# Kernel tuning notes

Measured on AMD Instinct MI355X. Metric: run time of the kernel, lower is better.

## Reference

```python
import jax, jax.numpy as jnp
import numpy as np

N = 100000; E = 800000; IN_DIM = 32; HID = 64; HEADS = 4; HEAD_DIM = HID // HEADS; L = 3; G = 128

def setup_inputs() -> dict:
    key = jax.random.key(0)
    ks = jax.random.split(key, 12)
    nrm = lambda k, shape: jax.random.normal(k, shape, jnp.float32) * 0.05
    return {
        "x": jax.random.normal(ks[0], (N, IN_DIM), jnp.float32),
        "edge_index": jax.random.randint(ks[1], (2, E), 0, N),
        "edge_attr": jax.random.normal(ks[2], (E, 1), jnp.float32),
        "batch": jnp.sort(jax.random.randint(ks[3], (N,), 0, G)),
        "in_W": nrm(ks[4], (IN_DIM, HID)), "in_b": jnp.zeros((HID,), jnp.float32),
        "in_ln_g": jnp.ones((HID,), jnp.float32), "in_ln_b": jnp.zeros((HID,), jnp.float32),
        "W_qkv": nrm(ks[5], (L, 3, HID, HID)), "b_qkv": jnp.zeros((L, 3, HID), jnp.float32),
        "W_edge": nrm(ks[6], (L, 1, HID)),
        "W_skip": nrm(ks[7], (L, HID, HID)), "b_skip": jnp.zeros((L, HID), jnp.float32),
        "W_beta": nrm(ks[8], (L, 3 * HID)),
        "ln_g": jnp.ones((L, HID), jnp.float32), "ln_b": jnp.zeros((L, HID), jnp.float32),
        "r1_W": nrm(ks[9], (2 * HID, HID)), "r1_b": jnp.zeros((HID,), jnp.float32),
        "r2_W": nrm(ks[10], (HID, HID // 2)), "r2_b": jnp.zeros((HID // 2,), jnp.float32),
        "r3_W": nrm(ks[11], (HID // 2, 1)), "r3_b": jnp.zeros((1,), jnp.float32),
    }

def _layer_norm(x, g, b, eps=1e-5):
    mu = x.mean(-1, keepdims=True)
    var = ((x - mu) ** 2).mean(-1, keepdims=True)
    return (x - mu) * jax.lax.rsqrt(var + eps) * g + b

def _gelu(x):
    return jax.nn.gelu(x, approximate=False)  # matches torch F.gelu default (erf)

def _forward(x, edge_attr, in_W, in_b, in_ln_g, in_ln_b, W_qkv, b_qkv, W_edge,
             W_skip, b_skip, W_beta, ln_g, ln_b, r1_W, r1_b, r2_W, r2_b, r3_W, r3_b,
             edge_index, batch):
    src, dst = edge_index[0], edge_index[1]  # message flows src -> dst
    n = x.shape[0]
    h = _layer_norm(_gelu(x @ in_W + in_b), in_ln_g, in_ln_b)
    scale = 1.0 / jnp.sqrt(jnp.float32(HEAD_DIM))
    for l in range(L):
        res = h
        q = (h @ W_qkv[l, 0] + b_qkv[l, 0]).reshape(n, HEADS, HEAD_DIM)
        k = (h @ W_qkv[l, 1] + b_qkv[l, 1]).reshape(n, HEADS, HEAD_DIM)
        v = (h @ W_qkv[l, 2] + b_qkv[l, 2]).reshape(n, HEADS, HEAD_DIM)
        e = (edge_attr @ W_edge[l]).reshape(-1, HEADS, HEAD_DIM)  # [E,H,C]
        ke = k[src] + e
        alpha = jnp.einsum("ehc,ehc->eh", q[dst], ke) * scale      # [E,H]
        amax = jax.ops.segment_max(alpha, dst, num_segments=n)
        ex = jnp.exp(alpha - amax[dst])
        den = jax.ops.segment_sum(ex, dst, num_segments=n)
        alpha = ex / (den[dst] + 1e-16)                            # PyG softmax eps
        msg = alpha[..., None] * (v[src] + e)
        out = jax.ops.segment_sum(msg, dst, num_segments=n).reshape(n, HID)
        x_r = h @ W_skip[l] + b_skip[l]
        beta = jax.nn.sigmoid(jnp.concatenate([out, x_r, out - x_r], -1) @ W_beta[l])  # [N]
        out = beta[:, None] * x_r + (1.0 - beta[:, None]) * out
        h = _layer_norm(_gelu(out) + res, ln_g[l], ln_b[l])
    cnt = jax.ops.segment_sum(jnp.ones((n,), h.dtype), batch, num_segments=G)
    gmean = jax.ops.segment_sum(h, batch, num_segments=G) / jnp.maximum(cnt, 1.0)[:, None]
    gmax = jax.ops.segment_max(h, batch, num_segments=G)
    rep = jnp.concatenate([gmean, gmax], -1)  # [G, 2*HID]
    rep = _gelu(rep @ r1_W + r1_b)
    rep = _gelu(rep @ r2_W + r2_b)
    return (rep @ r3_W + r3_b).reshape(-1)

def reference(x, edge_index, edge_attr, batch, in_W, in_b, in_ln_g, in_ln_b,
              W_qkv, b_qkv, W_edge, W_skip, b_skip, W_beta, ln_g, ln_b,
              r1_W, r1_b, r2_W, r2_b, r3_W, r3_b):
    return _forward(x, edge_attr, in_W, in_b, in_ln_g, in_ln_b, W_qkv, b_qkv, W_edge,
                    W_skip, b_skip, W_beta, ln_g, ln_b, r1_W, r1_b, r2_W, r2_b, r3_W, r3_b,
                    edge_index, batch)
```

## Files before the change

kernel.cpp:

```cpp
#include <hip/hip_runtime.h>
#include <hip/hip_fp16.h>
#include <math.h>
#include <float.h>

#define LAYERS 3
#define NGRAPH 128
#define NPB 1024
#define NBMAX 256

typedef __attribute__((ext_vector_type(8))) short bf16x8;
typedef __attribute__((ext_vector_type(4))) float f32x4;

union bfr { int4 i; bf16x8 b; };

__device__ __forceinline__ float gelu_f(float x) {
    return 0.5f * x * (1.0f + erff(x * 0.70710678118654752440f));
}

template <int CTRL, int RMASK>
__device__ __forceinline__ float dpp_add(float x) {
    int t = __builtin_amdgcn_update_dpp(0, __float_as_int(x), CTRL, RMASK, 0xF, false);
    return x + __int_as_float(t);
}

__device__ __forceinline__ float sum16(float v) {
    v = dpp_add<0xB1, 0xF>(v);
    v = dpp_add<0x4E, 0xF>(v);
    v = dpp_add<0x141, 0xF>(v);
    v = dpp_add<0x140, 0xF>(v);
    return v;
}

__device__ __forceinline__ unsigned int f2mono(float f) {
    unsigned int u = __float_as_uint(f);
    return (u & 0x80000000u) ? ~u : (u | 0x80000000u);
}
__device__ __forceinline__ float mono2f(unsigned int u) {
    return (u & 0x80000000u) ? __uint_as_float(u ^ 0x80000000u)
                             : __uint_as_float(~u);
}

__device__ __forceinline__ float2 h2f2(int bits) {
    __half2 h = *reinterpret_cast<__half2*>(&bits);
    return __half22float2(h);
}

__device__ __forceinline__ void cvt_frag(const float4& f0, const float4& f1,
                                         bf16x8& hi, bf16x8& lo) {
    float ff[8] = {f0.x, f0.y, f0.z, f0.w, f1.x, f1.y, f1.z, f1.w};
#pragma unroll
    for (int j = 0; j < 8; j++) {
        unsigned u = __float_as_uint(ff[j]);
        hi[j] = (short)(u >> 16);
        float hf = __uint_as_float(u & 0xFFFF0000u);
        lo[j] = (short)(__float_as_uint(ff[j] - hf) >> 16);
    }
}

__device__ __forceinline__ f32x4 mm3(const bf16x8& ahi, const bf16x8& alo,
                                     const int4* __restrict__ pk, int tile,
                                     int lane, f32x4 acc) {
    bfr bh, bl;
    bh.i = pk[tile * 128 + lane];
    bl.i = pk[tile * 128 + 64 + lane];
    acc = __builtin_amdgcn_mfma_f32_16x16x32_bf16(alo, bh.b, acc, 0, 0, 0);
    acc = __builtin_amdgcn_mfma_f32_16x16x32_bf16(ahi, bl.b, acc, 0, 0, 0);
    acc = __builtin_amdgcn_mfma_f32_16x16x32_bf16(ahi, bh.b, acc, 0, 0, 0);
    return acc;
}

__global__ __launch_bounds__(256) void k_cvt(
    const float* __restrict__ in_W, const float* __restrict__ W_skip,
    const float* __restrict__ W_qkv, int4* __restrict__ pk_in,
    int4* __restrict__ pk_skip, int4* __restrict__ pk_qkv) {
    int w = (blockIdx.x * 256 + threadIdx.x) >> 6;
    if (w >= 100) return;
    int lane = threadIdx.x & 63;
    const float* src;
    int4* dst;
    int kt, jt, qkvmode = 0;
    if (w < 4) {
        kt = 0; jt = w;
        src = in_W;
        dst = pk_in + w * 128;
    } else {
        int l = (w - 4) >> 5, r = (w - 4) & 31;
        if (r < 8) {
            kt = r & 1; jt = r >> 1;
            src = W_skip + l * 4096;
            dst = pk_skip + (l * 8 + r) * 128;
        } else {
            int tq = r - 8;
            kt = tq & 1; jt = tq >> 1;
            src = W_qkv + l * 12288;
            dst = pk_qkv + (l * 24 + tq) * 128;
            qkvmode = 1;
        }
    }
    int c = jt * 16 + (lane & 15);
    int koff = kt * 32 + (lane >> 4) * 8;
    unsigned hi[8], lo[8];
#pragma unroll
    for (int j = 0; j < 8; j++) {
        int k = koff + j;
        float f = qkvmode ? src[(c >> 6) * 4096 + k * 64 + (c & 63)]
                          : src[k * 64 + c];
        unsigned u = __float_as_uint(f);
        hi[j] = u >> 16;
        float hf = __uint_as_float(u & 0xFFFF0000u);
        lo[j] = __float_as_uint(f - hf) >> 16;
    }
    int4 H, L;
    H.x = hi[0] | (hi[1] << 16); H.y = hi[2] | (hi[3] << 16);
    H.z = hi[4] | (hi[5] << 16); H.w = hi[6] | (hi[7] << 16);
    L.x = lo[0] | (lo[1] << 16); L.y = lo[2] | (lo[3] << 16);
    L.z = lo[4] | (lo[5] << 16); L.w = lo[6] | (lo[7] << 16);
    dst[lane] = H;
    dst[64 + lane] = L;
}

__global__ __launch_bounds__(256) void k_hist(const int* __restrict__ dst,
                                              int* __restrict__ deg, int E) {
    int e = blockIdx.x * 256 + threadIdx.x;
    if (e < E) atomicAdd(&deg[dst[e]], 1);
}

__global__ __launch_bounds__(256) void k_scan1(const int* __restrict__ deg,
                                               int* __restrict__ excl,
                                               int* __restrict__ bsum, int n) {
    __shared__ int s[256];
    int t = threadIdx.x;
    int i = blockIdx.x * 256 + t;
    int v = (i < n) ? deg[i] : 0;
    s[t] = v;
    __syncthreads();
    for (int off = 1; off < 256; off <<= 1) {
        int a = (t >= off) ? s[t - off] : 0;
        __syncthreads();
        s[t] += a;
        __syncthreads();
    }
    if (i < n) excl[i] = s[t] - v;
    if (t == 255) bsum[blockIdx.x] = s[255];
}

__global__ __launch_bounds__(512) void k_scan2(int* __restrict__ bsum, int nb) {
    __shared__ int s[512];
    int t = threadIdx.x;
    int v = (t < nb) ? bsum[t] : 0;
    s[t] = v;
    __syncthreads();
    for (int off = 1; off < 512; off <<= 1) {
        int a = (t >= off) ? s[t - off] : 0;
        __syncthreads();
        s[t] += a;
        __syncthreads();
    }
    if (t < nb) bsum[t] = s[t] - v;
}

__global__ __launch_bounds__(256) void k_scan3(const int* __restrict__ excl,
                                               const int* __restrict__ bsum,
                                               int* __restrict__ row,
                                               int* __restrict__ cursor,
                                               int* __restrict__ gcurb,
                                               int n, int E) {
    int i = blockIdx.x * 256 + threadIdx.x;
    if (i < n) {
        int r = excl[i] + bsum[blockIdx.x];
        row[i] = r;
        cursor[i] = r;
        if ((i & (NPB - 1)) == 0) gcurb[i >> 10] = r;
    }
    if (blockIdx.x == 0 && threadIdx.x == 0) row[n] = E;
}

__global__ __launch_bounds__(256) void k_bucket(
    const int* __restrict__ src, const int* __restrict__ dst,
    const float* __restrict__ ea, int* __restrict__ gcurb,
    int2* __restrict__ mid, int E, int nbkt) {
    __shared__ int cnt[NBMAX], base_[NBMAX];
    int tile = blockIdx.x * 4096;
    for (int i = threadIdx.x; i < nbkt; i += 256) cnt[i] = 0;
    __syncthreads();
    int d[16];
#pragma unroll
    for (int j = 0; j < 16; j++) {
        int e = tile + j * 256 + threadIdx.x;
        d[j] = -1;
        if (e < E) {
            d[j] = dst[e];
            atomicAdd(&cnt[d[j] >> 10], 1);
        }
    }
    __syncthreads();
    for (int i = threadIdx.x; i < nbkt; i += 256) {
        base_[i] = atomicAdd(&gcurb[i], cnt[i]);
        cnt[i] = 0;
    }
    __syncthreads();
#pragma unroll
    for (int j = 0; j < 16; j++) {
        int e = tile + j * 256 + threadIdx.x;
        if (e < E) {
            int b = d[j] >> 10;
            int p = base_[b] + atomicAdd(&cnt[b], 1);
            mid[p] = make_int2(src[e] | ((d[j] & (NPB - 1)) << 20),
                               __float_as_int(ea[e]));
        }
    }
}

__global__ __launch_bounds__(256) void k_local(
    const int* __restrict__ row, int* __restrict__ cursor,
    const int2* __restrict__ mid, int2* __restrict__ ep, int n) {
    int b = blockIdx.x;
    int n0 = b << 10;
    int n1 = min(n, n0 + NPB);
    int ebeg = row[n0], eend = row[n1];
    for (int e = ebeg + blockIdx.y * 256 + threadIdx.x; e < eend;
         e += 256 * gridDim.y) {
        int2 m = mid[e];
        int dn = n0 + ((m.x >> 20) & (NPB - 1));
        int p = atomicAdd(&cursor[dn], 1);
        ep[p] = make_int2(m.x & 0xFFFFF, m.y);
    }
}

__device__ __forceinline__ int kv_idx(int m, int cc) {
    return (cc >> 2) * 8 + (m - 1) * 4 + (cc & 3);
}

__global__ __launch_bounds__(256) void k_in_qkv(
    const float* __restrict__ x, const int4* __restrict__ pk_in,
    const float* __restrict__ b, const float* __restrict__ g,
    const float* __restrict__ be, const int4* __restrict__ pk_qkv,
    const float* __restrict__ bn, float* __restrict__ h,
    __half* __restrict__ q, __half* __restrict__ kvout, int n) {
    __shared__ float lds[4][1088];
    int lane = threadIdx.x & 63, wid = threadIdx.x >> 6;
    int nb = (blockIdx.x * 4 + wid) * 16;
    if (nb >= n) return;
    int g16 = lane >> 4, c16 = lane & 15;
    int arow = min(nb + c16, n - 1);
    const float* xp = x + (size_t)arow * 32 + g16 * 8;
    float4 f0 = *(const float4*)xp;
    float4 f1 = *(const float4*)(xp + 4);
    bf16x8 ahi, alo;
    cvt_frag(f0, f1, ahi, alo);
    float gv[4][4];
#pragma unroll
    for (int jt = 0; jt < 4; jt++) {
        f32x4 a = {0.f, 0.f, 0.f, 0.f};
        a = mm3(ahi, alo, pk_in, jt, lane, a);
        float bb = b[jt * 16 + c16];
#pragma unroll
        for (int r = 0; r < 4; r++) gv[jt][r] = gelu_f(a[r] + bb);
    }
    float gl[4], bel[4];
#pragma unroll
    for (int jt = 0; jt < 4; jt++) {
        gl[jt] = g[jt * 16 + c16];
        bel[jt] = be[jt * 16 + c16];
    }
    float hreg[4][4];
#pragma unroll
    for (int r = 0; r < 4; r++) {
        float s = gv[0][r] + gv[1][r] + gv[2][r] + gv[3][r];
        float mu = sum16(s) * (1.0f / 64.0f);
        float vs = 0.f;
#pragma unroll
        for (int jt = 0; jt < 4; jt++) {
            float d = gv[jt][r] - mu;
            vs += d * d;
        }
        float var = sum16(vs) * (1.0f / 64.0f);
        float rs = rsqrtf(var + 1e-5f);
#pragma unroll
        for (int jt = 0; jt < 4; jt++)
            hreg[jt][r] = (gv[jt][r] - mu) * rs * gl[jt] + bel[jt];
    }
#pragma unroll
    for (int jt = 0; jt < 4; jt++)
#pragma unroll
        for (int r = 0; r < 4; r++) {
            int nd = nb + g16 * 4 + r;
            if (nd < n) h[(size_t)nd * 64 + jt * 16 + c16] = hreg[jt][r];
            lds[wid][(g16 * 4 + r) * 68 + jt * 16 + c16] = hreg[jt][r];
        }
    bf16x8 qahi[2], qalo[2];
#pragma unroll
    for (int kt = 0; kt < 2; kt++) {
        const float* lp = &lds[wid][c16 * 68 + kt * 32 + g16 * 8];
        float4 t0 = *(const float4*)lp;
        float4 t1 = *(const float4*)(lp + 4);
        cvt_frag(t0, t1, qahi[kt], qalo[kt]);
    }
#pragma unroll
    for (int jt = 0; jt < 12; jt++) {
        f32x4 a = {0.f, 0.f, 0.f, 0.f};
#pragma unroll
        for (int kt = 0; kt < 2; kt++) a = mm3(qahi[kt], qalo[kt], pk_qkv, jt * 2 + kt, lane, a);
        int c = jt * 16 + c16;
        float bias = bn[c];
        int m = c >> 6, cc = c & 63;
#pragma unroll
        for (int r = 0; r < 4; r++) {
            int nd = nb + g16 * 4 + r;
            if (nd < n) {
                float val = a[r] + bias;
                if (m == 0) q[(size_t)nd * 64 + cc] = __float2half(val);
                else kvout[(size_t)nd * 128 + kv_idx(m, cc)] = __float2half(val);
            }
        }
    }
}

__global__ __launch_bounds__(256) void k_attn(
    const __half* __restrict__ q, const __half* __restrict__ kv,
    const int* __restrict__ row, const int2* __restrict__ ep,
    const float* __restrict__ We, float* __restrict__ out, int n) {
    int lane = threadIdx.x & 63;
    int node = blockIdx.x * 4 + (threadIdx.x >> 6);
    if (node >= n) return;
    int g = lane >> 4;
    int c16 = lane & 15;
    int2 qb = *(const int2*)(q + (size_t)node * 64 + c16 * 4);
    float2 q01 = h2f2(qb.x), q23 = h2f2(qb.y);
    float4 wv = *(const float4*)(We + c16 * 4);
    int beg = row[node], end = row[node + 1];
    float den = 0.f;
    float4 acc = {0.f, 0.f, 0.f, 0.f};
    for (int pos = beg; pos < end; pos += 8) {
        int idx0 = pos + g, idx1 = pos + 4 + g;
        bool v0 = idx0 < end, v1 = idx1 < end;
        int2 pr0 = ep[v0 ? idx0 : beg];
        int2 pr1 = ep[v1 ? idx1 : beg];
        float a0 = __int_as_float(pr0.y), a1 = __int_as_float(pr1.y);
        int4 kb0 = *(const int4*)(kv + (size_t)pr0.x * 128 + c16 * 8);
        int4 kb1 = *(const int4*)(kv + (size_t)pr1.x * 128 + c16 * 8);
        {
            float2 k01 = h2f2(kb0.x), k23 = h2f2(kb0.y);
            float2 v01 = h2f2(kb0.z), v23 = h2f2(kb0.w);
            float p = q01.x * fmaf(a0, wv.x, k01.x) + q01.y * fmaf(a0, wv.y, k01.y) +
                      q23.x * fmaf(a0, wv.z, k23.x) + q23.y * fmaf(a0, wv.w, k23.y);
            p = dpp_add<0xB1, 0xF>(p);
            p = dpp_add<0x4E, 0xF>(p);
            float ex = v0 ? __expf(fminf(p * 0.25f, 60.f)) : 0.f;
            den += ex;
            acc.x = fmaf(ex, fmaf(a0, wv.x, v01.x), acc.x);
            acc.y = fmaf(ex, fmaf(a0, wv.y, v01.y), acc.y);
            acc.z = fmaf(ex, fmaf(a0, wv.z, v23.x), acc.z);
            acc.w = fmaf(ex, fmaf(a0, wv.w, v23.y), acc.w);
        }
        {
            float2 k01 = h2f2(kb1.x), k23 = h2f2(kb1.y);
            float2 v01 = h2f2(kb1.z), v23 = h2f2(kb1.w);
            float p = q01.x * fmaf(a1, wv.x, k01.x) + q01.y * fmaf(a1, wv.y, k01.y) +
                      q23.x * fmaf(a1, wv.z, k23.x) + q23.y * fmaf(a1, wv.w, k23.y);
            p = dpp_add<0xB1, 0xF>(p);
            p = dpp_add<0x4E, 0xF>(p);
            float ex = v1 ? __expf(fminf(p * 0.25f, 60.f)) : 0.f;
            den += ex;
            acc.x = fmaf(ex, fmaf(a1, wv.x, v01.x), acc.x);
            acc.y = fmaf(ex, fmaf(a1, wv.y, v01.y), acc.y);
            acc.z = fmaf(ex, fmaf(a1, wv.z, v23.x), acc.z);
            acc.w = fmaf(ex, fmaf(a1, wv.w, v23.y), acc.w);
        }
    }
#pragma unroll
    for (int mask = 16; mask <= 32; mask <<= 1) {
        den += __shfl_xor(den, mask, 64);
        acc.x += __shfl_xor(acc.x, mask, 64);
        acc.y += __shfl_xor(acc.y, mask, 64);
        acc.z += __shfl_xor(acc.z, mask, 64);
        acc.w += __shfl_xor(acc.w, mask, 64);
    }
    if (g == 0) {
        float inv = 1.0f / (den + 1e-16f);
        float4 o = {acc.x * inv, acc.y * inv, acc.z * inv, acc.w * inv};
        *(float4*)(out + (size_t)node * 64 + c16 * 4) = o;
    }
}

template <int DO_QKV>
__global__ __launch_bounds__(256) void k_node_qkv(
    float* __restrict__ h, const float* __restrict__ o_in,
    const int4* __restrict__ pk_skip, const float* __restrict__ bs,
    const float* __restrict__ Wb, const float* __restrict__ lg,
    const float* __restrict__ lb, const int4* __restrict__ pk_qkv,
    const float* __restrict__ bn, __half* __restrict__ q,
    __half* __restrict__ kvout, const int* __restrict__ batch,
    float* __restrict__ gsum, unsigned int* __restrict__ gmaxu,
    float* __restrict__ cnt, int n) {
    __shared__ float lds[4][DO_QKV ? 1088 : 4];
    int lane = threadIdx.x & 63, wid = threadIdx.x >> 6;
    int nb = (blockIdx.x * 4 + wid) * 16;
    if (nb >= n) return;
    int g16 = lane >> 4, c16 = lane & 15;
    bf16x8 ahi[2], alo[2];
    int arow = min(nb + c16, n - 1);
#pragma unroll
    for (int kt = 0; kt < 2; kt++) {
        const float* hp = h + (size_t)arow * 64 + kt * 32 + g16 * 8;
        float4 f0 = *(const float4*)hp;
        float4 f1 = *(const float4*)(hp + 4);
        cvt_frag(f0, f1, ahi[kt], alo[kt]);
    }
    float xr[4][4];
#pragma unroll
    for (int jt = 0; jt < 4; jt++) {
        f32x4 a = {0.f, 0.f, 0.f, 0.f};
#pragma unroll
        for (int kt = 0; kt < 2; kt++) a = mm3(ahi[kt], alo[kt], pk_skip, jt * 2 + kt, lane, a);
        float bias = bs[jt * 16 + c16];
#pragma unroll
        for (int r = 0; r < 4; r++) xr[jt][r] = a[r] + bias;
    }
    float ov[4][4], hold[4][4];
#pragma unroll
    for (int jt = 0; jt < 4; jt++)
#pragma unroll
        for (int r = 0; r < 4; r++) {
            int nd = min(nb + g16 * 4 + r, n - 1);
            ov[jt][r] = o_in[(size_t)nd * 64 + jt * 16 + c16];
            hold[jt][r] = h[(size_t)nd * 64 + jt * 16 + c16];
        }
    float wb0[4], wb1[4], wb2[4], lgv[4], lbv[4];
#pragma unroll
    for (int jt = 0; jt < 4; jt++) {
        int c = jt * 16 + c16;
        wb0[jt] = Wb[c]; wb1[jt] = Wb[64 + c]; wb2[jt] = Wb[128 + c];
        lgv[jt] = lg[c]; lbv[jt] = lb[c];
    }
    float hnew[4][4];
#pragma unroll
    for (int r = 0; r < 4; r++) {
        float cbs = 0.f;
#pragma unroll
        for (int jt = 0; jt < 4; jt++)
            cbs += ov[jt][r] * wb0[jt] + xr[jt][r] * wb1[jt] +
                   (ov[jt][r] - xr[jt][r]) * wb2[jt];
        float cb = sum16(cbs);
        float beta = 1.0f / (1.0f + expf(-cb));
        float gvr[4], s = 0.f;
#pragma unroll
        for (int jt = 0; jt < 4; jt++) {
            float o2 = fmaf(beta, xr[jt][r] - ov[jt][r], ov[jt][r]);
            gvr[jt] = gelu_f(o2) + hold[jt][r];
            s += gvr[jt];
        }
        float mu = sum16(s) * (1.0f / 64.0f);
        float vs = 0.f;
#pragma unroll
        for (int jt = 0; jt < 4; jt++) {
            float d = gvr[jt] - mu;
            vs += d * d;
        }
        float var = sum16(vs) * (1.0f / 64.0f);
        float rs = rsqrtf(var + 1e-5f);
#pragma unroll
        for (int jt = 0; jt < 4; jt++)
            hnew[jt][r] = (gvr[jt] - mu) * rs * lgv[jt] + lbv[jt];
    }
    if (DO_QKV) {
#pragma unroll
        for (int jt = 0; jt < 4; jt++)
#pragma unroll
            for (int r = 0; r < 4; r++) {
                int nd = nb + g16 * 4 + r;
                if (nd < n) h[(size_t)nd * 64 + jt * 16 + c16] = hnew[jt][r];
                lds[wid][(g16 * 4 + r) * 68 + jt * 16 + c16] = hnew[jt][r];
            }
        bf16x8 qahi[2], qalo[2];
#pragma unroll
        for (int kt = 0; kt < 2; kt++) {
            const float* lp = &lds[wid][c16 * 68 + kt * 32 + g16 * 8];
            float4 t0 = *(const float4*)lp;
            float4 t1 = *(const float4*)(lp + 4);
            cvt_frag(t0, t1, qahi[kt], qalo[kt]);
        }
#pragma unroll
        for (int jt = 0; jt < 12; jt++) {
            f32x4 a = {0.f, 0.f, 0.f, 0.f};
#pragma unroll
            for (int kt = 0; kt < 2; kt++) a = mm3(qahi[kt], qalo[kt], pk_qkv, jt * 2 + kt, lane, a);
            int c = jt * 16 + c16;
            float bias = bn[c];
            int m = c >> 6, cc = c & 63;
#pragma unroll
            for (int r = 0; r < 4; r++) {
                int nd = nb + g16 * 4 + r;
                if (nd < n) {
                    float val = a[r] + bias;
                    if (m == 0) q[(size_t)nd * 64 + cc] = __float2half(val);
                    else kvout[(size_t)nd * 128 + kv_idx(m, cc)] = __float2half(val);
                }
            }
        }
    } else {
        int gid[4];
        int g0 = batch[nb];
        bool ok = (nb + 15 < n);
#pragma unroll
        for (int r = 0; r < 4; r++)
            gid[r] = batch[min(nb + g16 * 4 + r, n - 1)];
        bool uni = ok && __all(gid[0] == g0 && gid[1] == g0 &&
                               gid[2] == g0 && gid[3] == g0);
        if (uni) {
            float s[4], mx[4];
#pragma unroll
            for (int jt = 0; jt < 4; jt++) {
                s[jt] = hnew[jt][0] + hnew[jt][1] + hnew[jt][2] + hnew[jt][3];
                mx[jt] = fmaxf(fmaxf(hnew[jt][0], hnew[jt][1]),
                               fmaxf(hnew[jt][2], hnew[jt][3]));
            }
#pragma unroll
            for (int mask = 16; mask <= 32; mask <<= 1) {
#pragma unroll
                for (int jt = 0; jt < 4; jt++) {
                    s[jt] += __shfl_xor(s[jt], mask, 64);
                    mx[jt] = fmaxf(mx[jt], __shfl_xor(mx[jt], mask, 64));
                }
            }
            if (g16 == 0) {
#pragma unroll
                for (int jt = 0; jt < 4; jt++) {
                    int ch = jt * 16 + c16;
                    atomicAdd(&gsum[g0 * 64 + ch], s[jt]);
                    atomicMax(&gmaxu[g0 * 64 + ch], f2mono(mx[jt]));
                }
            }
            if (lane == 0) atomicAdd(&cnt[g0], 16.0f);
        } else {
#pragma unroll
            for (int r = 0; r < 4; r++) {
                int nd = nb + g16 * 4 + r;
                if (nd >= n) continue;
#pragma unroll
                for (int jt = 0; jt < 4; jt++) {
                    int ch = jt * 16 + c16;
                    atomicAdd(&gsum[gid[r] * 64 + ch], hnew[jt][r]);
                    atomicMax(&gmaxu[gid[r] * 64 + ch], f2mono(hnew[jt][r]));
                }
                if (c16 == 0) atomicAdd(&cnt[gid[r]], 1.0f);
            }
        }
    }
}

__global__ void k_final(const float* __restrict__ gsum,
                        const unsigned int* __restrict__ gmax,
                        const float* __restrict__ cnt,
                        const float* __restrict__ W1, const float* __restrict__ b1,
                        const float* __restrict__ W2, const float* __restrict__ b2,
                        const float* __restrict__ W3, const float* __restrict__ b3,
                        float* __restrict__ out) {
    int g = blockIdx.x;
    int lane = threadIdx.x;
    __shared__ float rep[128];
    __shared__ float t1[64];
    __shared__ float t2[32];
    float c = fmaxf(cnt[g], 1.0f);
    rep[lane] = gsum[g * 64 + lane] / c;
    rep[64 + lane] = mono2f(gmax[g * 64 + lane]);
    __syncthreads();
    float a = b1[lane];
#pragma unroll 8
    for (int i = 0; i < 128; i++) a = fmaf(rep[i], W1[i * 64 + lane], a);
    t1[lane] = gelu_f(a);
    __syncthreads();
    if (lane < 32) {
        float a2 = b2[lane];
#pragma unroll 8
        for (int i = 0; i < 64; i++) a2 = fmaf(t1[i], W2[i * 32 + lane], a2);
        t2[lane] = gelu_f(a2);
    }
    __syncthreads();
    if (lane < 32) {
        float p = t2[lane] * W3[lane];
#pragma unroll
        for (int o = 16; o > 0; o >>= 1) p += __shfl_xor(p, o, 64);
        if (lane == 0) out[g] = p + b3[0];
    }
}

extern "C" void kernel_launch(void* const* d_in, const int* in_sizes, int n_in,
                              void* d_out, int out_size, void* d_ws,
                              size_t ws_size, hipStream_t stream) {
    const float* x      = (const float*)d_in[0];
    const int*   eidx   = (const int*)d_in[1];
    const float* ea     = (const float*)d_in[2];
    const int*   batch  = (const int*)d_in[3];
    const float* in_W   = (const float*)d_in[4];
    const float* in_b   = (const float*)d_in[5];
    const float* in_lng = (const float*)d_in[6];
    const float* in_lnb = (const float*)d_in[7];
    const float* W_qkv  = (const float*)d_in[8];
    const float* b_qkv  = (const float*)d_in[9];
    const float* W_edge = (const float*)d_in[10];
    const float* W_skip = (const float*)d_in[11];
    const float* b_skip = (const float*)d_in[12];
    const float* W_beta = (const float*)d_in[13];
    const float* ln_g   = (const float*)d_in[14];
    const float* ln_b   = (const float*)d_in[15];
    const float* r1_W   = (const float*)d_in[16];
    const float* r1_b   = (const float*)d_in[17];
    const float* r2_W   = (const float*)d_in[18];
    const float* r2_b   = (const float*)d_in[19];
    const float* r3_W   = (const float*)d_in[20];
    const float* r3_b   = (const float*)d_in[21];

    int n = in_sizes[0] / 32;
    int E = in_sizes[2];
    const int* src = eidx;
    const int* dst = eidx + E;

    char* ws = (char*)d_ws;
    size_t off = 0;
    auto alloc = [&](size_t bytes) -> void* {
        void* p = ws + off;
        off = (off + bytes + 255) & ~(size_t)255;
        return p;
    };
    float* h    = (float*)alloc((size_t)n * 64 * 4);
    __half* qh  = (__half*)alloc((size_t)n * 64 * 2);
    __half* kvh = (__half*)alloc((size_t)n * 128 * 2);
    float* oacc = (float*)alloc((size_t)n * 64 * 4);
    int* deg    = (int*)alloc((size_t)n * 4);
    int* excl   = (int*)alloc((size_t)n * 4);
    int* bsum   = (int*)alloc(512 * 4);
    int* row    = (int*)alloc((size_t)(n + 1) * 4);
    int* cursor = (int*)alloc((size_t)n * 4);
    int* gcurb  = (int*)alloc(NBMAX * 4);
    int2* mid   = (int2*)alloc((size_t)E * 8);
    int2* ep    = (int2*)alloc((size_t)E * 8);
    int4* pk_in   = (int4*)alloc(4 * 128 * 16);
    int4* pk_skip = (int4*)alloc(3 * 8 * 128 * 16);
    int4* pk_qkv  = (int4*)alloc((size_t)3 * 24 * 128 * 16);
    float* gsum = (float*)alloc((NGRAPH * 64 * 2 + NGRAPH) * 4);
    unsigned int* gmaxu = (unsigned int*)(gsum + NGRAPH * 64);
    float* cnt  = gsum + NGRAPH * 128;

    int nb4 = (n + 3) / 4;
    int nb64 = (n + 63) / 64;
    int nbs = (n + 255) / 256;
    int ebs = (E + 255) / 256;
    int nbkt = (n + NPB - 1) >> 10;

    k_cvt<<<25, 256, 0, stream>>>(in_W, W_skip, W_qkv, pk_in, pk_skip, pk_qkv);
    hipMemsetAsync(deg, 0, (size_t)n * 4, stream);
    hipMemsetAsync(gsum, 0, (NGRAPH * 64 * 2 + NGRAPH) * 4, stream);
    k_hist<<<ebs, 256, 0, stream>>>(dst, deg, E);
    k_scan1<<<nbs, 256, 0, stream>>>(deg, excl, bsum, n);
    k_scan2<<<1, 512, 0, stream>>>(bsum, nbs);
    k_scan3<<<nbs, 256, 0, stream>>>(excl, bsum, row, cursor, gcurb, n, E);
    k_bucket<<<(E + 4095) / 4096, 256, 0, stream>>>(src, dst, ea, gcurb, mid, E, nbkt);
    k_local<<<dim3(nbkt, 4), 256, 0, stream>>>(row, cursor, mid, ep, n);

    k_in_qkv<<<nb64, 256, 0, stream>>>(x, pk_in, in_b, in_lng, in_lnb,
                                       pk_qkv, b_qkv, h, qh, kvh, n);

    for (int l = 0; l < LAYERS; l++) {
        k_attn<<<nb4, 256, 0, stream>>>(qh, kvh, row, ep, W_edge + l * 64, oacc, n);
        if (l + 1 < LAYERS) {
            k_node_qkv<1><<<nb64, 256, 0, stream>>>(
                h, oacc, pk_skip + l * 8 * 128, b_skip + l * 64,
                W_beta + l * 192, ln_g + l * 64, ln_b + l * 64,
                pk_qkv + (size_t)(l + 1) * 24 * 128, b_qkv + (size_t)(l + 1) * 192,
                qh, kvh, nullptr, nullptr, nullptr, nullptr, n);
        } else {
            k_node_qkv<0><<<nb64, 256, 0, stream>>>(
                h, oacc, pk_skip + l * 8 * 128, b_skip + l * 64,
                W_beta + l * 192, ln_g + l * 64, ln_b + l * 64,
                nullptr, nullptr, nullptr, nullptr,
                batch, gsum, gmaxu, cnt, n);
        }
    }

    k_final<<<NGRAPH, 64, 0, stream>>>(gsum, gmaxu, cnt, r1_W, r1_b, r2_W, r2_b,
                                       r3_W, r3_b, (float*)d_out);
}
```

Before: 381.1 us.

## Process 4 nodes per 64-thread block in node kernels and hoist edge term in attention

The node-side kernels (input projection and per-layer skip/beta/LN/QKV) now launch one 64-thread block per 4 nodes instead of 256-thread blocks covering 64 nodes. Only 4 of the 16 MFMA rows carry real nodes, and results are staged through LDS so that h, q and kv are written with coalesced vector stores instead of scattered half stores. This spreads the node work over many more small blocks and cleans up the store pattern, but three quarters of the MFMA rows do redundant work and an extra block-level sync is added. Separately, the attention kernel folds the edge-attribute term algebraically: q·W_edge is computed once per node and the sum of exp-weighted edge attributes is accumulated, which removes per-edge FMAs.

```diff
diff --git a/kernel.cpp b/kernel.cpp
--- a/kernel.cpp
+++ b/kernel.cpp
@@ -28,6 +28,11 @@
     v = dpp_add<0x4E, 0xF>(v);
     v = dpp_add<0x141, 0xF>(v);
     v = dpp_add<0x140, 0xF>(v);
+    return v;
+}
+__device__ __forceinline__ float sum4(float v) {
+    v = dpp_add<0xB1, 0xF>(v);
+    v = dpp_add<0x4E, 0xF>(v);
     return v;
 }
 
@@ -67,6 +72,10 @@
     acc = __builtin_amdgcn_mfma_f32_16x16x32_bf16(ahi, bl.b, acc, 0, 0, 0);
     acc = __builtin_amdgcn_mfma_f32_16x16x32_bf16(ahi, bh.b, acc, 0, 0, 0);
     return acc;
+}
+
+__device__ __forceinline__ int kv_idx(int m, int cc) {
+    return (cc >> 2) * 8 + (m - 1) * 4 + (cc & 3);
 }
 
 __global__ __launch_bounds__(256) void k_cvt(
@@ -227,93 +236,111 @@
     }
 }
 
-__device__ __forceinline__ int kv_idx(int m, int cc) {
-    return (cc >> 2) * 8 + (m - 1) * 4 + (cc & 3);
-}
-
-__global__ __launch_bounds__(256) void k_in_qkv(
+__device__ __forceinline__ void qkv_gemm_store(
+    const float* ldsH, float* ldsQf, const int4* __restrict__ pk_qkv,
+    const float* __restrict__ bn, __half* __restrict__ q,
+    __half* __restrict__ kvout, int nb, int n, int lane, int g16, int c16) {
+    bf16x8 qahi[2], qalo[2];
+#pragma unroll
+    for (int kt = 0; kt < 2; kt++) {
+        const float* lp = &ldsH[(c16 & 3) * 64 + kt * 32 + g16 * 8];
+        float4 t0 = *(const float4*)lp;
+        float4 t1 = *(const float4*)(lp + 4);
+        cvt_frag(t0, t1, qahi[kt], qalo[kt]);
+    }
+    __half* ldsQh = reinterpret_cast<__half*>(ldsQf);
+#pragma unroll
+    for (int jt = 0; jt < 12; jt++) {
+        f32x4 a = {0.f, 0.f, 0.f, 0.f};
+#pragma unroll
+        for (int kt = 0; kt < 2; kt++)
+            a = mm3(qahi[kt], qalo[kt], pk_qkv, jt * 2 + kt, lane, a);
+        int c = jt * 16 + c16;
+        float bias = bn[c];
+        int m = c >> 6, cc = c & 63;
+        int colpos = (m == 0) ? cc : (64 + kv_idx(m, cc));
+        if (g16 == 0) {
+#pragma unroll
+            for (int r = 0; r < 4; r++)
+                ldsQh[r * 200 + colpos] = __float2half(a[r] + bias);
+        }
+    }
+    __syncthreads();
+    if (lane < 32) {
+        int row = lane >> 3, ck = lane & 7;
+        if (nb + row < n)
+            *(int4*)(q + (size_t)(nb + row) * 64 + ck * 8) =
+                *(const int4*)&ldsQh[row * 200 + ck * 8];
+    }
+    {
+        int row = lane >> 4, ck = lane & 15;
+        if (nb + row < n)
+            *(int4*)(kvout + (size_t)(nb + row) * 128 + ck * 8) =
+                *(const int4*)&ldsQh[row * 200 + 64 + ck * 8];
+    }
+}
+
+__global__ __launch_bounds__(64) void k_in_qkv4(
     const float* __restrict__ x, const int4* __restrict__ pk_in,
     const float* __restrict__ b, const float* __restrict__ g,
     const float* __restrict__ be, const int4* __restrict__ pk_qkv,
     const float* __restrict__ bn, float* __restrict__ h,
     __half* __restrict__ q, __half* __restrict__ kvout, int n) {
-    __shared__ float lds[4][1088];
-    int lane = threadIdx.x & 63, wid = threadIdx.x >> 6;
-    int nb = (blockIdx.x * 4 + wid) * 16;
+    __shared__ __align__(16) float ldsH[256];
+    __shared__ __align__(16) float ldsX[256];
+    __shared__ __align__(16) float ldsQf[4][100];
+    int lane = threadIdx.x;
+    int nb = blockIdx.x * 4;
     if (nb >= n) return;
     int g16 = lane >> 4, c16 = lane & 15;
-    int arow = min(nb + c16, n - 1);
+    int arow = min(nb + (c16 & 3), n - 1);
     const float* xp = x + (size_t)arow * 32 + g16 * 8;
     float4 f0 = *(const float4*)xp;
     float4 f1 = *(const float4*)(xp + 4);
     bf16x8 ahi, alo;
     cvt_frag(f0, f1, ahi, alo);
-    float gv[4][4];
 #pragma unroll
     for (int jt = 0; jt < 4; jt++) {
         f32x4 a = {0.f, 0.f, 0.f, 0.f};
         a = mm3(ahi, alo, pk_in, jt, lane, a);
-        float bb = b[jt * 16 + c16];
-#pragma unroll
-        for (int r = 0; r < 4; r++) gv[jt][r] = gelu_f(a[r] + bb);
-    }
-    float gl[4], bel[4];
-#pragma unroll
-    for (int jt = 0; jt < 4; jt++) {
-        gl[jt] = g[jt * 16 + c16];
-        bel[jt] = be[jt * 16 + c16];
-    }
-    float hreg[4][4];
-#pragma unroll
-    for (int r = 0; r < 4; r++) {
-        float s = gv[0][r] + gv[1][r] + gv[2][r] + gv[3][r];
-        float mu = sum16(s) * (1.0f / 64.0f);
-        float vs = 0.f;
-#pragma unroll
-        for (int jt = 0; jt < 4; jt++) {
-            float d = gv[jt][r] - mu;
-            vs += d * d;
-        }
-        float var = sum16(vs) * (1.0f / 64.0f);
-        float rs = rsqrtf(var + 1e-5f);
-#pragma unroll
-        for (int jt = 0; jt < 4; jt++)
-            hreg[jt][r] = (gv[jt][r] - mu) * rs * gl[jt] + bel[jt];
-    }
-#pragma unroll
-    for (int jt = 0; jt < 4; jt++)
-#pragma unroll
-        for (int r = 0; r < 4; r++) {
-            int nd = nb + g16 * 4 + r;
-            if (nd < n) h[(size_t)nd * 64 + jt * 16 + c16] = hreg[jt][r];
-            lds[wid][(g16 * 4 + r) * 68 + jt * 16 + c16] = hreg[jt][r];
-        }
-    bf16x8 qahi[2], qalo[2];
-#pragma unroll
-    for (int kt = 0; kt < 2; kt++) {
-        const float* lp = &lds[wid][c16 * 68 + kt * 32 + g16 * 8];
-        float4 t0 = *(const float4*)lp;
-        float4 t1 = *(const float4*)(lp + 4);
-        cvt_frag(t0, t1, qahi[kt], qalo[kt]);
-    }
-#pragma unroll
-    for (int jt = 0; jt < 12; jt++) {
-        f32x4 a = {0.f, 0.f, 0.f, 0.f};
-#pragma unroll
-        for (int kt = 0; kt < 2; kt++) a = mm3(qahi[kt], qalo[kt], pk_qkv, jt * 2 + kt, lane, a);
-        int c = jt * 16 + c16;
-        float bias = bn[c];
-        int m = c >> 6, cc = c & 63;
-#pragma unroll
-        for (int r = 0; r < 4; r++) {
-            int nd = nb + g16 * 4 + r;
-            if (nd < n) {
-                float val = a[r] + bias;
-                if (m == 0) q[(size_t)nd * 64 + cc] = __float2half(val);
-                else kvout[(size_t)nd * 128 + kv_idx(m, cc)] = __float2half(val);
-            }
-        }
-    }
+        float bias = b[jt * 16 + c16];
+        if (g16 == 0) {
+#pragma unroll
+            for (int r = 0; r < 4; r++)
+                ldsX[r * 64 + jt * 16 + c16] = a[r] + bias;
+        }
+    }
+    __syncthreads();
+    float gv[4];
+    float ssum = 0.f;
+#pragma unroll
+    for (int jj = 0; jj < 4; jj++) {
+        gv[jj] = gelu_f(ldsX[g16 * 64 + jj * 16 + c16]);
+        ssum += gv[jj];
+    }
+    float mu = sum16(ssum) * (1.0f / 64.0f);
+    float vs = 0.f;
+#pragma unroll
+    for (int jj = 0; jj < 4; jj++) {
+        float d = gv[jj] - mu;
+        vs += d * d;
+    }
+    float var = sum16(vs) * (1.0f / 64.0f);
+    float rs = rsqrtf(var + 1e-5f);
+#pragma unroll
+    for (int jj = 0; jj < 4; jj++) {
+        int ch = jj * 16 + c16;
+        float hn = (gv[jj] - mu) * rs * g[ch] + be[ch];
+        ldsH[g16 * 64 + ch] = hn;
+    }
+    __syncthreads();
+    {
+        int row = g16, ck = c16;
+        if (nb + row < n)
+            *(float4*)(h + (size_t)(nb + row) * 64 + ck * 4) =
+                *(const float4*)&ldsH[row * 64 + ck * 4];
+    }
+    qkv_gemm_store(ldsH, &ldsQf[0][0], pk_qkv, bn, q, kvout, nb, n, lane, g16, c16);
 }
 
 __global__ __launch_bounds__(256) void k_attn(
@@ -328,8 +355,9 @@
     int2 qb = *(const int2*)(q + (size_t)node * 64 + c16 * 4);
     float2 q01 = h2f2(qb.x), q23 = h2f2(qb.y);
     float4 wv = *(const float4*)(We + c16 * 4);
+    float qwe = sum4(q01.x * wv.x + q01.y * wv.y + q23.x * wv.z + q23.y * wv.w);
     int beg = row[node], end = row[node + 1];
-    float den = 0.f;
+    float den = 0.f, aes = 0.f;
     float4 acc = {0.f, 0.f, 0.f, 0.f};
     for (int pos = beg; pos < end; pos += 8) {
         int idx0 = pos + g, idx1 = pos + 4 + g;
@@ -342,35 +370,34 @@
         {
             float2 k01 = h2f2(kb0.x), k23 = h2f2(kb0.y);
             float2 v01 = h2f2(kb0.z), v23 = h2f2(kb0.w);
-            float p = q01.x * fmaf(a0, wv.x, k01.x) + q01.y * fmaf(a0, wv.y, k01.y) +
-                      q23.x * fmaf(a0, wv.z, k23.x) + q23.y * fmaf(a0, wv.w, k23.y);
-            p = dpp_add<0xB1, 0xF>(p);
-            p = dpp_add<0x4E, 0xF>(p);
-            float ex = v0 ? __expf(fminf(p * 0.25f, 60.f)) : 0.f;
+            float p = q01.x * k01.x + q01.y * k01.y + q23.x * k23.x + q23.y * k23.y;
+            p = sum4(p);
+            float ex = v0 ? __expf(fminf(fmaf(a0, qwe, p) * 0.25f, 60.f)) : 0.f;
             den += ex;
-            acc.x = fmaf(ex, fmaf(a0, wv.x, v01.x), acc.x);
-            acc.y = fmaf(ex, fmaf(a0, wv.y, v01.y), acc.y);
-            acc.z = fmaf(ex, fmaf(a0, wv.z, v23.x), acc.z);
-            acc.w = fmaf(ex, fmaf(a0, wv.w, v23.y), acc.w);
+            aes = fmaf(ex, a0, aes);
+            acc.x = fmaf(ex, v01.x, acc.x);
+            acc.y = fmaf(ex, v01.y, acc.y);
+            acc.z = fmaf(ex, v23.x, acc.z);
+            acc.w = fmaf(ex, v23.y, acc.w);
         }
         {
             float2 k01 = h2f2(kb1.x), k23 = h2f2(kb1.y);
             float2 v01 = h2f2(kb1.z), v23 = h2f2(kb1.w);
-            float p = q01.x * fmaf(a1, wv.x, k01.x) + q01.y * fmaf(a1, wv.y, k01.y) +
-                      q23.x * fmaf(a1, wv.z, k23.x) + q23.y * fmaf(a1, wv.w, k23.y);
-            p = dpp_add<0xB1, 0xF>(p);
-            p = dpp_add<0x4E, 0xF>(p);
-            float ex = v1 ? __expf(fminf(p * 0.25f, 60.f)) : 0.f;
+            float p = q01.x * k01.x + q01.y * k01.y + q23.x * k23.x + q23.y * k23.y;
+            p = sum4(p);
+            float ex = v1 ? __expf(fminf(fmaf(a1, qwe, p) * 0.25f, 60.f)) : 0.f;
             den += ex;
-            acc.x = fmaf(ex, fmaf(a1, wv.x, v01.x), acc.x);
-            acc.y = fmaf(ex, fmaf(a1, wv.y, v01.y), acc.y);
-            acc.z = fmaf(ex, fmaf(a1, wv.z, v23.x), acc.z);
-            acc.w = fmaf(ex, fmaf(a1, wv.w, v23.y), acc.w);
+            aes = fmaf(ex, a1, aes);
+            acc.x = fmaf(ex, v01.x, acc.x);
+            acc.y = fmaf(ex, v01.y, acc.y);
+            acc.z = fmaf(ex, v23.x, acc.z);
+            acc.w = fmaf(ex, v23.y, acc.w);
         }
     }
 #pragma unroll
     for (int mask = 16; mask <= 32; mask <<= 1) {
         den += __shfl_xor(den, mask, 64);
+        aes += __shfl_xor(aes, mask, 64);
         acc.x += __shfl_xor(acc.x, mask, 64);
         acc.y += __shfl_xor(acc.y, mask, 64);
         acc.z += __shfl_xor(acc.z, mask, 64);
@@ -378,13 +405,17 @@
     }
     if (g == 0) {
         float inv = 1.0f / (den + 1e-16f);
-        float4 o = {acc.x * inv, acc.y * inv, acc.z * inv, acc.w * inv};
+        float4 o;
+        o.x = fmaf(aes, wv.x, acc.x) * inv;
+        o.y = fmaf(aes, wv.y, acc.y) * inv;
+        o.z = fmaf(aes, wv.z, acc.z) * inv;
+        o.w = fmaf(aes, wv.w, acc.w) * inv;
         *(float4*)(out + (size_t)node * 64 + c16 * 4) = o;
     }
 }
 
 template <int DO_QKV>
-__global__ __launch_bounds__(256) void k_node_qkv(
+__global__ __launch_bounds__(64) void k_node_qkv4(
     float* __restrict__ h, const float* __restrict__ o_in,
     const int4* __restrict__ pk_skip, const float* __restrict__ bs,
     const float* __restrict__ Wb, const float* __restrict__ lg,
@@ -393,157 +424,119 @@
     __half* __restrict__ kvout, const int* __restrict__ batch,
     float* __restrict__ gsum, unsigned int* __restrict__ gmaxu,
     float* __restrict__ cnt, int n) {
-    __shared__ float lds[4][DO_QKV ? 1088 : 4];
-    int lane = threadIdx.x & 63, wid = threadIdx.x >> 6;
-    int nb = (blockIdx.x * 4 + wid) * 16;
+    __shared__ __align__(16) float ldsH[256];
+    __shared__ __align__(16) float ldsX[256];
+    __shared__ __align__(16) float ldsQf[4][100];
+    int lane = threadIdx.x;
+    int nb = blockIdx.x * 4;
     if (nb >= n) return;
     int g16 = lane >> 4, c16 = lane & 15;
+    int myn = min(nb + g16, n - 1);
+    int arow = min(nb + (c16 & 3), n - 1);
+    const float* hp = h + (size_t)arow * 64 + g16 * 8;
+    float4 hf0 = *(const float4*)hp;
+    float4 hf1 = *(const float4*)(hp + 4);
+    float4 hf2 = *(const float4*)(hp + 32);
+    float4 hf3 = *(const float4*)(hp + 36);
+    float ov[4], hold[4];
+#pragma unroll
+    for (int jj = 0; jj < 4; jj++) {
+        ov[jj] = o_in[(size_t)myn * 64 + jj * 16 + c16];
+        hold[jj] = h[(size_t)myn * 64 + jj * 16 + c16];
+    }
     bf16x8 ahi[2], alo[2];
-    int arow = min(nb + c16, n - 1);
-#pragma unroll
-    for (int kt = 0; kt < 2; kt++) {
-        const float* hp = h + (size_t)arow * 64 + kt * 32 + g16 * 8;
-        float4 f0 = *(const float4*)hp;
-        float4 f1 = *(const float4*)(hp + 4);
-        cvt_frag(f0, f1, ahi[kt], alo[kt]);
-    }
-    float xr[4][4];
+    cvt_frag(hf0, hf1, ahi[0], alo[0]);
+    cvt_frag(hf2, hf3, ahi[1], alo[1]);
 #pragma unroll
     for (int jt = 0; jt < 4; jt++) {
         f32x4 a = {0.f, 0.f, 0.f, 0.f};
 #pragma unroll
-        for (int kt = 0; kt < 2; kt++) a = mm3(ahi[kt], alo[kt], pk_skip, jt * 2 + kt, lane, a);
+        for (int kt = 0; kt < 2; kt++)
+            a = mm3(ahi[kt], alo[kt], pk_skip, jt * 2 + kt, lane, a);
         float bias = bs[jt * 16 + c16];
-#pragma unroll
-        for (int r = 0; r < 4; r++) xr[jt][r] = a[r] + bias;
-    }
-    float ov[4][4], hold[4][4];
-#pragma unroll
-    for (int jt = 0; jt < 4; jt++)
-#pragma unroll
-        for (int r = 0; r < 4; r++) {
-            int nd = min(nb + g16 * 4 + r, n - 1);
-            ov[jt][r] = o_in[(size_t)nd * 64 + jt * 16 + c16];
-            hold[jt][r] = h[(size_t)nd * 64 + jt * 16 + c16];
-        }
-    float wb0[4], wb1[4], wb2[4], lgv[4], lbv[4];
-#pragma unroll
-    for (int jt = 0; jt < 4; jt++) {
-        int c = jt * 16 + c16;
-        wb0[jt] = Wb[c]; wb1[jt] = Wb[64 + c]; wb2[jt] = Wb[128 + c];
-        lgv[jt] = lg[c]; lbv[jt] = lb[c];
-    }
-    float hnew[4][4];
-#pragma unroll
-    for (int r = 0; r < 4; r++) {
-        float cbs = 0.f;
-#pragma unroll
-        for (int jt = 0; jt < 4; jt++)
-            cbs += ov[jt][r] * wb0[jt] + xr[jt][r] * wb1[jt] +
-                   (ov[jt][r] - xr[jt][r]) * wb2[jt];
-        float cb = sum16(cbs);
-        float beta = 1.0f / (1.0f + expf(-cb));
-        float gvr[4], s = 0.f;
-#pragma unroll
-        for (int jt = 0; jt < 4; jt++) {
-            float o2 = fmaf(beta, xr[jt][r] - ov[jt][r], ov[jt][r]);
-            gvr[jt] = gelu_f(o2) + hold[jt][r];
-            s += gvr[jt];
-        }
-        float mu = sum16(s) * (1.0f / 64.0f);
-        float vs = 0.f;
-#pragma unroll
-        for (int jt = 0; jt < 4; jt++) {
-            float d = gvr[jt] - mu;
-            vs += d * d;
-        }
-        float var = sum16(vs) * (1.0f / 64.0f);
-        float rs = rsqrtf(var + 1e-5f);
-#pragma unroll
-        for (int jt = 0; jt < 4; jt++)
-            hnew[jt][r] = (gvr[jt] - mu) * rs * lgv[jt] + lbv[jt];
-    }
+        if (g16 == 0) {
+#pragma unroll
+            for (int r = 0; r < 4; r++)
+                ldsX[r * 64 + jt * 16 + c16] = a[r] + bias;
+        }
+    }
+    __syncthreads();
+    float xr[4], wb0[4], wb1[4], wb2[4], lgv[4], lbv[4];
+#pragma unroll
+    for (int jj = 0; jj < 4; jj++) {
+        int ch = jj * 16 + c16;
+        xr[jj] = ldsX[g16 * 64 + ch];
+        wb0[jj] = Wb[ch]; wb1[jj] = Wb[64 + ch]; wb2[jj] = Wb[128 + ch];
+        lgv[jj] = lg[ch]; lbv[jj] = lb[ch];
+    }
+    float cbs = 0.f;
+#pragma unroll
+    for (int jj = 0; jj < 4; jj++)
+        cbs += ov[jj] * wb0[jj] + xr[jj] * wb1[jj] + (ov[jj] - xr[jj]) * wb2[jj];
+    float cb = sum16(cbs);
+    float beta = 1.0f / (1.0f + expf(-cb));
+    float gvr[4], ssum = 0.f;
+#pragma unroll
+    for (int jj = 0; jj < 4; jj++) {
+        float o2 = fmaf(beta, xr[jj] - ov[jj], ov[jj]);
+        gvr[jj] = gelu_f(o2) + hold[jj];
+        ssum += gvr[jj];
+    }
+    float mu = sum16(ssum) * (1.0f / 64.0f);
+    float vs = 0.f;
+#pragma unroll
+    for (int jj = 0; jj < 4; jj++) {
+        float d = gvr[jj] - mu;
+        vs += d * d;
+    }
+    float var = sum16(vs) * (1.0f / 64.0f);
+    float rs = rsqrtf(var + 1e-5f);
+    float hnew[4];
+#pragma unroll
+    for (int jj = 0; jj < 4; jj++)
+        hnew[jj] = (gvr[jj] - mu) * rs * lgv[jj] + lbv[jj];
     if (DO_QKV) {
 #pragma unroll
-        for (int jt = 0; jt < 4; jt++)
-#pragma unroll
-            for (int r = 0; r < 4; r++) {
-                int nd = nb + g16 * 4 + r;
-                if (nd < n) h[(size_t)nd * 64 + jt * 16 + c16] = hnew[jt][r];
-                lds[wid][(g16 * 4 + r) * 68 + jt * 16 + c16] = hnew[jt][r];
-            }
-        bf16x8 qahi[2], qalo[2];
-#pragma unroll
-        for (int kt = 0; kt < 2; kt++) {
-            const float* lp = &lds[wid][c16 * 68 + kt * 32 + g16 * 8];
-            float4 t0 = *(const float4*)lp;
-            float4 t1 = *(const float4*)(lp + 4);
-            cvt_frag(t0, t1, qahi[kt], qalo[kt]);
-        }
-#pragma unroll
-        for (int jt = 0; jt < 12; jt++) {
-            f32x4 a = {0.f, 0.f, 0.f, 0.f};
-#pragma unroll
-            for (int kt = 0; kt < 2; kt++) a = mm3(qahi[kt], qalo[kt], pk_qkv, jt * 2 + kt, lane, a);
-            int c = jt * 16 + c16;
-            float bias = bn[c];
-            int m = c >> 6, cc = c & 63;
-#pragma unroll
-            for (int r = 0; r < 4; r++) {
-                int nd = nb + g16 * 4 + r;
-                if (nd < n) {
-                    float val = a[r] + bias;
-                    if (m == 0) q[(size_t)nd * 64 + cc] = __float2half(val);
-                    else kvout[(size_t)nd * 128 + kv_idx(m, cc)] = __float2half(val);
+        for (int jj = 0; jj < 4; jj++)
+            ldsH[g16 * 64 + jj * 16 + c16] = hnew[jj];
+        __syncthreads();
+        {
+            int row = g16, ck = c16;
+            if (nb + row < n)
+                *(float4*)(h + (size_t)(nb + row) * 64 + ck * 4) =
+                    *(const float4*)&ldsH[row * 64 + ck * 4];
+        }
+        qkv_gemm_store(ldsH, &ldsQf[0][0], pk_qkv, bn, q, kvout, nb, n, lane, g16, c16);
+    } else {
+        int gid = batch[myn];
+        int g0 = batch[nb];
+        bool allok = (nb + 3 < n);
+        bool uni = allok && __all(gid == g0);
+        if (uni) {
+#pragma unroll
+            for (int jj = 0; jj < 4; jj++) {
+                float s = hnew[jj];
+                float mx = hnew[jj];
+                s += __shfl_xor(s, 16, 64);
+                s += __shfl_xor(s, 32, 64);
+                mx = fmaxf(mx, __shfl_xor(mx, 16, 64));
+                mx = fmaxf(mx, __shfl_xor(mx, 32, 64));
+                if (g16 == 0) {
+                    int ch = jj * 16 + c16;
+                    atomicAdd(&gsum[g0 * 64 + ch], s);
+                    atomicMax(&gmaxu[g0 * 64 + ch], f2mono(mx));
                 }
             }
-        }
-    } else {
-        int gid[4];
-        int g0 = batch[nb];
-        bool ok = (nb + 15 < n);
-#pragma unroll
-        for (int r = 0; r < 4; r++)
-            gid[r] = batch[min(nb + g16 * 4 + r, n - 1)];
-        bool uni = ok && __all(gid[0] == g0 && gid[1] == g0 &&
-                               gid[2] == g0 && gid[3] == g0);
-        if (uni) {
-            float s[4], mx[4];
-#pragma unroll
-            for (int jt = 0; jt < 4; jt++) {
-                s[jt] = hnew[jt][0] + hnew[jt][1] + hnew[jt][2] + hnew[jt][3];
-                mx[jt] = fmaxf(fmaxf(hnew[jt][0], hnew[jt][1]),
-                               fmaxf(hnew[jt][2], hnew[jt][3]));
-            }
-#pragma unroll
-            for (int mask = 16; mask <= 32; mask <<= 1) {
-#pragma unroll
-                for (int jt = 0; jt < 4; jt++) {
-                    s[jt] += __shfl_xor(s[jt], mask, 64);
-                    mx[jt] = fmaxf(mx[jt], __shfl_xor(mx[jt], mask, 64));
+            if (lane == 0) atomicAdd(&cnt[g0], 4.0f);
+        } else {
+            if (nb + g16 < n) {
+#pragma unroll
+                for (int jj = 0; jj < 4; jj++) {
+                    int ch = jj * 16 + c16;
+                    atomicAdd(&gsum[gid * 64 + ch], hnew[jj]);
+                    atomicMax(&gmaxu[gid * 64 + ch], f2mono(hnew[jj]));
                 }
-            }
-            if (g16 == 0) {
-#pragma unroll
-                for (int jt = 0; jt < 4; jt++) {
-                    int ch = jt * 16 + c16;
-                    atomicAdd(&gsum[g0 * 64 + ch], s[jt]);
-                    atomicMax(&gmaxu[g0 * 64 + ch], f2mono(mx[jt]));
-                }
-            }
-            if (lane == 0) atomicAdd(&cnt[g0], 16.0f);
-        } else {
-#pragma unroll
-            for (int r = 0; r < 4; r++) {
-                int nd = nb + g16 * 4 + r;
-                if (nd >= n) continue;
-#pragma unroll
-                for (int jt = 0; jt < 4; jt++) {
-                    int ch = jt * 16 + c16;
-                    atomicAdd(&gsum[gid[r] * 64 + ch], hnew[jt][r]);
-                    atomicMax(&gmaxu[gid[r] * 64 + ch], f2mono(hnew[jt][r]));
-                }
-                if (c16 == 0) atomicAdd(&cnt[gid[r]], 1.0f);
+                if (c16 == 0) atomicAdd(&cnt[gid], 1.0f);
             }
         }
     }
@@ -643,7 +636,6 @@
     float* cnt  = gsum + NGRAPH * 128;
 
     int nb4 = (n + 3) / 4;
-    int nb64 = (n + 63) / 64;
     int nbs = (n + 255) / 256;
     int ebs = (E + 255) / 256;
     int nbkt = (n + NPB - 1) >> 10;
@@ -658,20 +650,20 @@
     k_bucket<<<(E + 4095) / 4096, 256, 0, stream>>>(src, dst, ea, gcurb, mid, E, nbkt);
     k_local<<<dim3(nbkt, 4), 256, 0, stream>>>(row, cursor, mid, ep, n);
 
-    k_in_qkv<<<nb64, 256, 0, stream>>>(x, pk_in, in_b, in_lng, in_lnb,
-                                       pk_qkv, b_qkv, h, qh, kvh, n);
+    k_in_qkv4<<<nb4, 64, 0, stream>>>(x, pk_in, in_b, in_lng, in_lnb,
+                                      pk_qkv, b_qkv, h, qh, kvh, n);
 
     for (int l = 0; l < LAYERS; l++) {
         k_attn<<<nb4, 256, 0, stream>>>(qh, kvh, row, ep, W_edge + l * 64, oacc, n);
         if (l + 1 < LAYERS) {
-            k_node_qkv<1><<<nb64, 256, 0, stream>>>(
-                h, oacc, pk_skip + l * 8 * 128, b_skip + l * 64,
+            k_node_qkv4<1><<<nb4, 64, 0, stream>>>(
+                h, oacc, pk_skip + l * 1024, b_skip + l * 64,
                 W_beta + l * 192, ln_g + l * 64, ln_b + l * 64,
-                pk_qkv + (size_t)(l + 1) * 24 * 128, b_qkv + (size_t)(l + 1) * 192,
+                pk_qkv + (size_t)(l + 1) * 3072, b_qkv + (size_t)(l + 1) * 192,
                 qh, kvh, nullptr, nullptr, nullptr, nullptr, n);
         } else {
-            k_node_qkv<0><<<nb64, 256, 0, stream>>>(
-                h, oacc, pk_skip + l * 8 * 128, b_skip + l * 64,
+            k_node_qkv4<0><<<nb4, 64, 0, stream>>>(
+                h, oacc, pk_skip + l * 1024, b_skip + l * 64,
                 W_beta + l * 192, ln_g + l * 64, ln_b + l * 64,
                 nullptr, nullptr, nullptr, nullptr,
                 batch, gsum, gmaxu, cnt, n);
```

Result: slower. 585.5 us, median of 4 (+53.7%).
